# Kernel tuning notes

Hardware: AMD Instinct MI355X
Metric: run time of the kernel (lower is better)

The kernel has to match this reference:

```python
import jax, jax.numpy as jnp
from jax import lax
import numpy as np

REACH = 4
NPRED = 4
NBINS = 256


def _conv(x, w, groups=1):
    # NCHW valid conv
    return lax.conv_general_dilated(
        x, w, window_strides=(1, 1), padding='VALID',
        dimension_numbers=('NCHW', 'OIHW', 'NCHW'),
        feature_group_count=groups)


def _median3(a, b, c):
    return jnp.maximum(jnp.minimum(a, jnp.maximum(b, c)), jnp.minimum(b, c))


def _calc_rmse(x):
    return 255.0 * jnp.sqrt(jnp.mean(jnp.square(x)))


def _calc_invCR(x):
    # torch.histc(x, 256, -1, 1) per (batch, channel) slice, then Shannon entropy
    b, c, h, w = x.shape
    nch = b * c
    res = h * w
    xf = x.reshape(nch, res)
    valid = ((xf >= -1.0) & (xf <= 1.0)).astype(jnp.float32)  # histc ignores out-of-range
    idx = jnp.clip(jnp.floor((xf + 1.0) * (NBINS / 2.0)).astype(jnp.int32), 0, NBINS - 1)
    flat = (jnp.arange(nch, dtype=jnp.int32)[:, None] * NBINS + idx).reshape(-1)
    counts = jnp.zeros(nch * NBINS, jnp.float32).at[flat].add(valid.reshape(-1))
    prob = counts / res
    ent = jnp.sum(jnp.where(prob > 0, -prob * jnp.log2(jnp.where(prob > 0, prob, 1.0)), 0.0))
    return ent / (8.0 * nch)


def _forward(x, w0T, w0L, b0L, w1, b1, w2, b2):
    r, g, b = x[:, 0:1], x[:, 1:2], x[:, 2:3]
    yuv = jnp.concatenate([r - g, g, b - g], axis=1)  # [B,3,H,W]
    # conv0T: causal-north context, pad (left=4, right=4, top=4) on rows [:-1]
    padT = jnp.pad(yuv[:, :, :-1, :], ((0, 0), (0, 0), (REACH, 0), (REACH, REACH)))
    # conv0L: causal-west context, pad left=4 on cols [:-1]
    padL = jnp.pad(yuv[:, :, :, :-1], ((0, 0), (0, 0), (0, 0), (REACH, 0)))
    pred = jax.nn.leaky_relu(_conv(padT, w0T) + _conv(padL, w0L) + b0L[None, :, None, None])
    # grouped 1x1 mixing back to 3 channels (conv1, conv2; groups=3)
    pred = jax.nn.leaky_relu(_conv(pred, w1, groups=3) + b1[None, :, None, None])
    pred = _conv(pred, w2, groups=3) + b2[None, :, None, None]  # [B,3,H,W]
    north = jnp.pad(yuv[:, :, :-1, :], ((0, 0), (0, 0), (1, 0), (0, 0)))
    west = jnp.pad(yuv[:, :, :, :-1], ((0, 0), (0, 0), (0, 0), (1, 0)))
    northeast = jnp.pad(yuv[:, :, :-1, 1:], ((0, 0), (0, 0), (1, 0), (0, 1)))
    vmin = jnp.minimum(west, jnp.minimum(north, northeast))
    vmax = jnp.maximum(west, jnp.maximum(north, northeast))
    pred = _median3(pred, vmin, vmax)
    pcr, py, pcb = pred[:, 0:1], pred[:, 1:2], pred[:, 2:3]
    pred = jnp.concatenate([pcr + g, py, pcb + g], axis=1)
    pred = jnp.clip(pred, -1.0, 1.0)
    delta = x - pred
    return delta


def setup_inputs() -> dict:
    key = jax.random.key(0)
    ks = jax.random.split(key, 9)
    B, H, W = 16, 512, 512
    x = jax.random.uniform(ks[0], (B, 3, H, W), jnp.float32) * 2.0 - 1.0
    s = 0.05
    return {
        'x': x,
        'w0T': jax.random.normal(ks[1], (3 * NPRED, 3, REACH, 2 * REACH + 1), jnp.float32) * s,
        'w0L': jax.random.normal(ks[2], (3 * NPRED, 3, 1, REACH), jnp.float32) * s,
        'b0L': jax.random.normal(ks[3], (3 * NPRED,), jnp.float32) * s,
        'w1': jax.random.normal(ks[4], (3 * NPRED, NPRED, 1, 1), jnp.float32) * s,
        'b1': jax.random.normal(ks[5], (3 * NPRED,), jnp.float32) * s,
        'w2': jax.random.normal(ks[6], (3, NPRED, 1, 1), jnp.float32) * s,
        'b2': jax.random.normal(ks[7], (3,), jnp.float32) * s,
    }


def reference(x, w0T, w0L, b0L, w1, b1, w2, b2):
    delta = _forward(x, w0T, w0L, b0L, w1, b1, w2, b2)
    loss1 = _calc_rmse(delta)
    loss0 = _calc_rmse(x)
    invCR0 = _calc_invCR(x)
    invCR1 = _calc_invCR(jnp.fmod(delta + 1.0, 2.0) - 1.0)
    return (loss1, loss0, invCR0, invCR1)
```

## Files before the change

### kernel.cpp

```cpp
#include <hip/hip_runtime.h>
#include <math.h>

constexpr int TH = 16, TW = 64;
constexpr int LH = TH + 4, LW = TW + 8;

typedef __attribute__((ext_vector_type(8))) short bf16x8;
typedef __attribute__((ext_vector_type(4))) float f32x4;

__device__ __forceinline__ float leaky(float v){ return v >= 0.0f ? v : 0.01f * v; }

__device__ __forceinline__ unsigned cvt_pk_bf16(float lo, float hi){
  unsigned r;
  asm("v_cvt_pk_bf16_f32 %0, %1, %2" : "=v"(r) : "v"(lo), "v"(hi));
  return r;
}

__global__ void codec_zero(unsigned int* ws, int n){
  int i = blockIdx.x * 256 + threadIdx.x;
  if (i < n) ws[i] = 0u;
}

__global__ __launch_bounds__(256) void codec_main(
    const float* __restrict__ x,
    const float* __restrict__ w0T, const float* __restrict__ w0L,
    const float* __restrict__ b0L,
    const float* __restrict__ w1, const float* __restrict__ b1,
    const float* __restrict__ w2, const float* __restrict__ b2,
    unsigned int* __restrict__ histX, unsigned int* __restrict__ histD,
    float* __restrict__ sums)
{
  __shared__ float yuv[3][LH][LW];
  __shared__ __attribute__((aligned(16))) float h0buf[4][4][16][16];
  __shared__ unsigned int lhX[3][256];
  __shared__ unsigned int lhD[3][256];
  __shared__ float red[2];

  const int tid  = threadIdx.x;
  const int lane = tid & 63;
  const int wv   = tid >> 6;
  const int p    = lane & 15;
  const int g    = lane >> 4;

  const int b  = blockIdx.z;
  const int h0 = blockIdx.y * TH;
  const int w0 = blockIdx.x * TW;

  bf16x8 afrag[4];
  #pragma unroll
  for (int t = 0; t < 4; ++t){
    float wv8[8];
    #pragma unroll
    for (int e = 0; e < 8; ++e){
      float v = 0.0f;
      if (p < 12){
        if (t < 3)          v = w0T[p*108 + t*36 + g*9 + e];
        else if (g < 3)     v = (e < 4) ? w0L[p*12 + g*4 + e]
                                        : w0T[p*108 + g*36 + (e-4)*9 + 8];
      }
      wv8[e] = v;
    }
    union { unsigned u[4]; bf16x8 s; } pk;
    #pragma unroll
    for (int i = 0; i < 4; ++i) pk.u[i] = cvt_pk_bf16(wv8[2*i], wv8[2*i+1]);
    afrag[t] = pk.s;
  }

  for (int i = tid; i < 3*256; i += 256){ (&lhX[0][0])[i] = 0u; (&lhD[0][0])[i] = 0u; }
  if (tid < 2) red[tid] = 0.0f;

  const float* xb = x + (size_t)b * (3*512*512);
  for (int i = tid; i < LH*LW; i += 256){
    int lr = i / LW, lc = i % LW;
    int h = h0 + lr - 4, w = w0 + lc - 4;
    float r = 0.f, gg = 0.f, bb = 0.f;
    if (h >= 0 && w >= 0 && w < 512){
      int off = h*512 + w;
      r  = xb[off];
      gg = xb[262144 + off];
      bb = xb[524288 + off];
    }
    yuv[0][lr][lc] = r - gg;
    yuv[1][lr][lc] = gg;
    yuv[2][lr][lc] = bb - gg;
  }
  __syncthreads();

  float lsq_d = 0.0f, lsq_x = 0.0f;

  for (int qi = 0; qi < 4; ++qi){
    const int row = wv*4 + qi;
    const int lr  = row + 4;

    for (int s = 0; s < 4; ++s){
      const int lc = 4 + s*16 + p;
      f32x4 acc = {0.f, 0.f, 0.f, 0.f};
      #pragma unroll
      for (int t = 0; t < 4; ++t){
        float f[8];
        if (t < 3){
          const float* src = &yuv[t][lr-4+g][lc-4];
          #pragma unroll
          for (int i = 0; i < 8; ++i) f[i] = src[i];
        } else {
          const int ic = (g < 3) ? g : 2;
          const float* L = &yuv[ic][lr][lc-4];
          #pragma unroll
          for (int i = 0; i < 4; ++i) f[i] = L[i];
          #pragma unroll
          for (int dy = 0; dy < 4; ++dy) f[4+dy] = yuv[ic][lr-4+dy][lc+4];
        }
        union { unsigned u[4]; bf16x8 s_; } pk;
        #pragma unroll
        for (int i = 0; i < 4; ++i) pk.u[i] = cvt_pk_bf16(f[2*i], f[2*i+1]);
        acc = __builtin_amdgcn_mfma_f32_16x16x32_bf16(afrag[t], pk.s_, acc, 0, 0, 0);
      }
      *(f32x4*)&h0buf[wv][s][p][g*4] = acc;
    }

    const int colp = lane;
    const int lc2  = colp + 4;
    f32x4 r0 = *(const f32x4*)&h0buf[wv][colp>>4][colp&15][0];
    f32x4 r1 = *(const f32x4*)&h0buf[wv][colp>>4][colp&15][4];
    f32x4 r2 = *(const f32x4*)&h0buf[wv][colp>>4][colp&15][8];
    float h0v[12] = { r0[0], r0[1], r0[2], r0[3],
                      r1[0], r1[1], r1[2], r1[3],
                      r2[0], r2[1], r2[2], r2[3] };
    #pragma unroll
    for (int oc = 0; oc < 12; ++oc) h0v[oc] = leaky(h0v[oc] + b0L[oc]);

    float h1v[12];
    #pragma unroll
    for (int j = 0; j < 12; ++j){
      int gsel = (j >> 2) << 2;
      float sv = b1[j];
      #pragma unroll
      for (int k = 0; k < 4; ++k) sv = fmaf(w1[j*4+k], h0v[gsel+k], sv);
      h1v[j] = leaky(sv);
    }
    float pr2[3];
    #pragma unroll
    for (int c = 0; c < 3; ++c){
      float sv = b2[c];
      #pragma unroll
      for (int k = 0; k < 4; ++k) sv = fmaf(w2[c*4+k], h1v[c*4+k], sv);
      pr2[c] = sv;
    }

    const float gpix = yuv[1][lr][lc2];
    const int h = h0 + row;
    const int w = w0 + colp;
    const int off = h*512 + w;

    #pragma unroll
    for (int c = 0; c < 3; ++c){
      float n  = yuv[c][lr-1][lc2];
      float wl = yuv[c][lr][lc2-1];
      float ne = yuv[c][lr-1][lc2+1];
      float vmin = fminf(wl, fminf(n, ne));
      float vmax = fmaxf(wl, fmaxf(n, ne));
      float pv = fminf(fmaxf(pr2[c], vmin), vmax);
      pv = (c == 1) ? pv : pv + gpix;
      pv = fminf(fmaxf(pv, -1.0f), 1.0f);

      float xv = xb[c*262144 + off];
      float d  = xv - pv;
      lsq_d = fmaf(d, d, lsq_d);
      lsq_x = fmaf(xv, xv, lsq_x);

      int ix = (int)floorf((xv + 1.0f) * 128.0f);
      ix = ix < 0 ? 0 : (ix > 255 ? 255 : ix);
      if (xv >= -1.0f && xv <= 1.0f) atomicAdd(&lhX[c][ix], 1u);

      float wd = fmodf(d + 1.0f, 2.0f) - 1.0f;
      int id = (int)floorf((wd + 1.0f) * 128.0f);
      id = id < 0 ? 0 : (id > 255 ? 255 : id);
      if (wd >= -1.0f && wd <= 1.0f) atomicAdd(&lhD[c][id], 1u);
    }
  }

  #pragma unroll
  for (int sft = 32; sft > 0; sft >>= 1){
    lsq_d += __shfl_down(lsq_d, sft);
    lsq_x += __shfl_down(lsq_x, sft);
  }
  if ((tid & 63) == 0){ atomicAdd(&red[0], lsq_d); atomicAdd(&red[1], lsq_x); }
  __syncthreads();
  if (tid == 0){ atomicAdd(&sums[0], red[0]); atomicAdd(&sums[1], red[1]); }

  for (int i = tid; i < 3*256; i += 256){
    int c = i >> 8, bin = i & 255;
    unsigned vX = lhX[c][bin];
    if (vX) atomicAdd(&histX[(b*3 + c)*256 + bin], vX);
    unsigned vD = lhD[c][bin];
    if (vD) atomicAdd(&histD[(b*3 + c)*256 + bin], vD);
  }
}

__global__ __launch_bounds__(256) void codec_final(
    const unsigned int* __restrict__ histX,
    const unsigned int* __restrict__ histD,
    const float* __restrict__ sums,
    float* __restrict__ out)
{
  __shared__ float se[2];
  if (threadIdx.x < 2) se[threadIdx.x] = 0.0f;
  __syncthreads();
  float eX = 0.0f, eD = 0.0f;
  for (int i = threadIdx.x; i < 48*256; i += 256){
    float pX = (float)histX[i] * (1.0f/262144.0f);
    if (pX > 0.0f) eX -= pX * log2f(pX);
    float pD = (float)histD[i] * (1.0f/262144.0f);
    if (pD > 0.0f) eD -= pD * log2f(pD);
  }
  #pragma unroll
  for (int s = 32; s > 0; s >>= 1){
    eX += __shfl_down(eX, s);
    eD += __shfl_down(eD, s);
  }
  if ((threadIdx.x & 63) == 0){ atomicAdd(&se[0], eX); atomicAdd(&se[1], eD); }
  __syncthreads();
  if (threadIdx.x == 0){
    out[0] = 255.0f * sqrtf(sums[0] * (1.0f/12582912.0f));
    out[1] = 255.0f * sqrtf(sums[1] * (1.0f/12582912.0f));
    out[2] = se[0] * (1.0f/384.0f);
    out[3] = se[1] * (1.0f/384.0f);
  }
}

extern "C" void kernel_launch(void* const* d_in, const int* in_sizes, int n_in,
                              void* d_out, int out_size, void* d_ws, size_t ws_size,
                              hipStream_t stream) {
  const float* x   = (const float*)d_in[0];
  const float* w0T = (const float*)d_in[1];
  const float* w0L = (const float*)d_in[2];
  const float* b0L = (const float*)d_in[3];
  const float* w1  = (const float*)d_in[4];
  const float* b1  = (const float*)d_in[5];
  const float* w2  = (const float*)d_in[6];
  const float* b2  = (const float*)d_in[7];

  unsigned int* histX = (unsigned int*)d_ws;
  unsigned int* histD = histX + 48*256;
  float* sums = (float*)(histD + 48*256);
  float* out = (float*)d_out;

  const int nzero = 48*256*2 + 2;
  codec_zero<<<(nzero + 255)/256, 256, 0, stream>>>((unsigned int*)d_ws, nzero);

  dim3 grid(512/TW, 512/TH, 16);
  codec_main<<<grid, 256, 0, stream>>>(x, w0T, w0L, b0L, w1, b1, w2, b2,
                                       histX, histD, sums);
  codec_final<<<1, 256, 0, stream>>>(histX, histD, sums, out);
}
```

Baseline: 239.3 us.

## Pre-pack bf16 tile pairs in LDS and run epilogue directly from MFMA accumulators

Adds a shared-memory pass that converts the YUV tile to packed bf16 pairs, one copy per column parity, so MFMA B-fragments become four dword loads instead of eight float loads plus conversions. The h0buf round-trip through LDS is removed: each MFMA output lane group now holds exactly one channel's four hidden values and finishes the grouped 1x1 mixes, median clamp, loss and histogram work itself. Per-group weights are hoisted into registers. The costs are an extra LDS conversion pass and sync, and a quarter of the lanes (g==3) sit idle during the epilogue.

```diff
diff --git a/kernel.cpp b/kernel.cpp
--- a/kernel.cpp
+++ b/kernel.cpp
@@ -3,6 +3,10 @@
 
 constexpr int TH = 16, TW = 64;
 constexpr int LH = TH + 4, LW = TW + 8;
+constexpr int PLS = LH*LW + 8;
+constexpr int PKW = LW/2;
+constexpr int PKPL = LH*PKW;
+constexpr int PKPAR = 3*PKPL;
 
 typedef __attribute__((ext_vector_type(8))) short bf16x8;
 typedef __attribute__((ext_vector_type(4))) float f32x4;
@@ -29,8 +33,8 @@
     unsigned int* __restrict__ histX, unsigned int* __restrict__ histD,
     float* __restrict__ sums)
 {
-  __shared__ float yuv[3][LH][LW];
-  __shared__ __attribute__((aligned(16))) float h0buf[4][4][16][16];
+  __shared__ float yuvF[3*PLS];
+  __shared__ unsigned pkF[2*PKPAR];
   __shared__ unsigned int lhX[3][256];
   __shared__ unsigned int lhD[3][256];
   __shared__ float red[2];
@@ -40,10 +44,13 @@
   const int wv   = tid >> 6;
   const int p    = lane & 15;
   const int g    = lane >> 4;
+  const int gg   = (g < 3) ? g : 0;
 
   const int b  = blockIdx.z;
   const int h0 = blockIdx.y * TH;
   const int w0 = blockIdx.x * TW;
+
+#define YUV(t, r, c) yuvF[(t)*PLS + (r)*LW + (c)]
 
   bf16x8 afrag[4];
   #pragma unroll
@@ -65,6 +72,19 @@
     afrag[t] = pk.s;
   }
 
+  float b0g[4], b1g[4], w2g[4], w1g[4][4];
+  #pragma unroll
+  for (int k = 0; k < 4; ++k){
+    b0g[k] = b0L[4*gg + k];
+    b1g[k] = b1[4*gg + k];
+    w2g[k] = w2[gg*4 + k];
+  }
+  #pragma unroll
+  for (int jj = 0; jj < 4; ++jj)
+    #pragma unroll
+    for (int k = 0; k < 4; ++k) w1g[jj][k] = w1[(4*gg + jj)*4 + k];
+  const float b2g = b2[gg];
+
   for (int i = tid; i < 3*256; i += 256){ (&lhX[0][0])[i] = 0u; (&lhD[0][0])[i] = 0u; }
   if (tid < 2) red[tid] = 0.0f;
 
@@ -72,16 +92,26 @@
   for (int i = tid; i < LH*LW; i += 256){
     int lr = i / LW, lc = i % LW;
     int h = h0 + lr - 4, w = w0 + lc - 4;
-    float r = 0.f, gg = 0.f, bb = 0.f;
+    float r = 0.f, ggv = 0.f, bb = 0.f;
     if (h >= 0 && w >= 0 && w < 512){
       int off = h*512 + w;
-      r  = xb[off];
-      gg = xb[262144 + off];
-      bb = xb[524288 + off];
+      r   = xb[off];
+      ggv = xb[262144 + off];
+      bb  = xb[524288 + off];
     }
-    yuv[0][lr][lc] = r - gg;
-    yuv[1][lr][lc] = gg;
-    yuv[2][lr][lc] = bb - gg;
+    YUV(0, lr, lc) = r - ggv;
+    YUV(1, lr, lc) = ggv;
+    YUV(2, lr, lc) = bb - ggv;
+  }
+  __syncthreads();
+
+  for (int i = tid; i < 2*PKPAR; i += 256){
+    int par = i / PKPAR, rem = i % PKPAR;
+    int pl = rem / PKPL, r2 = (rem % PKPL) / PKW, wd = rem % PKW;
+    int c0 = 2*wd + par, c1 = c0 + 1;
+    float lo = YUV(pl, r2, c0);
+    float hi = (c1 < LW) ? YUV(pl, r2, c1) : 0.0f;
+    pkF[i] = cvt_pk_bf16(lo, hi);
   }
   __syncthreads();
 
@@ -92,89 +122,72 @@
     const int lr  = row + 4;
 
     for (int s = 0; s < 4; ++s){
-      const int lc = 4 + s*16 + p;
+      const int c0    = s*16 + p;
+      const int par   = c0 & 1;
+      const int wbase = (c0 - par) >> 1;
       f32x4 acc = {0.f, 0.f, 0.f, 0.f};
+
       #pragma unroll
       for (int t = 0; t < 4; ++t){
-        float f[8];
+        union { unsigned u[4]; bf16x8 v; } B;
         if (t < 3){
-          const float* src = &yuv[t][lr-4+g][lc-4];
+          const unsigned* src = &pkF[par*PKPAR + t*PKPL + (lr-4+g)*PKW + wbase];
           #pragma unroll
-          for (int i = 0; i < 8; ++i) f[i] = src[i];
+          for (int i = 0; i < 4; ++i) B.u[i] = src[i];
         } else {
           const int ic = (g < 3) ? g : 2;
-          const float* L = &yuv[ic][lr][lc-4];
+          const unsigned* L = &pkF[par*PKPAR + ic*PKPL + lr*PKW + wbase];
+          B.u[0] = L[0]; B.u[1] = L[1];
+          float f4 = YUV(ic, lr-4+0, c0+8);
+          float f5 = YUV(ic, lr-4+1, c0+8);
+          float f6 = YUV(ic, lr-4+2, c0+8);
+          float f7 = YUV(ic, lr-4+3, c0+8);
+          B.u[2] = cvt_pk_bf16(f4, f5);
+          B.u[3] = cvt_pk_bf16(f6, f7);
+        }
+        acc = __builtin_amdgcn_mfma_f32_16x16x32_bf16(afrag[t], B.v, acc, 0, 0, 0);
+      }
+
+      if (g < 3){
+        const int lc = c0 + 4;
+        float h0v[4], h1v[4];
+        #pragma unroll
+        for (int k = 0; k < 4; ++k) h0v[k] = leaky(acc[k] + b0g[k]);
+        #pragma unroll
+        for (int jj = 0; jj < 4; ++jj){
+          float sv = b1g[jj];
           #pragma unroll
-          for (int i = 0; i < 4; ++i) f[i] = L[i];
-          #pragma unroll
-          for (int dy = 0; dy < 4; ++dy) f[4+dy] = yuv[ic][lr-4+dy][lc+4];
+          for (int k = 0; k < 4; ++k) sv = fmaf(w1g[jj][k], h0v[k], sv);
+          h1v[jj] = leaky(sv);
         }
-        union { unsigned u[4]; bf16x8 s_; } pk;
+        float pr = b2g;
         #pragma unroll
-        for (int i = 0; i < 4; ++i) pk.u[i] = cvt_pk_bf16(f[2*i], f[2*i+1]);
-        acc = __builtin_amdgcn_mfma_f32_16x16x32_bf16(afrag[t], pk.s_, acc, 0, 0, 0);
+        for (int k = 0; k < 4; ++k) pr = fmaf(w2g[k], h1v[k], pr);
+
+        float n  = YUV(g, lr-1, lc);
+        float wl = YUV(g, lr,   lc-1);
+        float ne = YUV(g, lr-1, lc+1);
+        float vmin = fminf(wl, fminf(n, ne));
+        float vmax = fmaxf(wl, fmaxf(n, ne));
+        float pv = fminf(fmaxf(pr, vmin), vmax);
+        float gpix = YUV(1, lr, lc);
+        pv = (g == 1) ? pv : pv + gpix;
+        pv = fminf(fmaxf(pv, -1.0f), 1.0f);
+
+        float xv = xb[g*262144 + (h0+row)*512 + (w0 + s*16 + p)];
+        float d  = xv - pv;
+        lsq_d = fmaf(d, d, lsq_d);
+        lsq_x = fmaf(xv, xv, lsq_x);
+
+        int ix = (int)floorf((xv + 1.0f) * 128.0f);
+        ix = ix < 0 ? 0 : (ix > 255 ? 255 : ix);
+        if (xv >= -1.0f && xv <= 1.0f) atomicAdd(&lhX[g][ix], 1u);
+
+        float wd2 = fmodf(d + 1.0f, 2.0f) - 1.0f;
+        int id = (int)floorf((wd2 + 1.0f) * 128.0f);
+        id = id < 0 ? 0 : (id > 255 ? 255 : id);
+        if (wd2 >= -1.0f && wd2 <= 1.0f) atomicAdd(&lhD[g][id], 1u);
       }
-      *(f32x4*)&h0buf[wv][s][p][g*4] = acc;
-    }
-
-    const int colp = lane;
-    const int lc2  = colp + 4;
-    f32x4 r0 = *(const f32x4*)&h0buf[wv][colp>>4][colp&15][0];
-    f32x4 r1 = *(const f32x4*)&h0buf[wv][colp>>4][colp&15][4];
-    f32x4 r2 = *(const f32x4*)&h0buf[wv][colp>>4][colp&15][8];
-    float h0v[12] = { r0[0], r0[1], r0[2], r0[3],
-                      r1[0], r1[1], r1[2], r1[3],
-                      r2[0], r2[1], r2[2], r2[3] };
-    #pragma unroll
-    for (int oc = 0; oc < 12; ++oc) h0v[oc] = leaky(h0v[oc] + b0L[oc]);
-
-    float h1v[12];
-    #pragma unroll
-    for (int j = 0; j < 12; ++j){
-      int gsel = (j >> 2) << 2;
-      float sv = b1[j];
-      #pragma unroll
-      for (int k = 0; k < 4; ++k) sv = fmaf(w1[j*4+k], h0v[gsel+k], sv);
-      h1v[j] = leaky(sv);
-    }
-    float pr2[3];
-    #pragma unroll
-    for (int c = 0; c < 3; ++c){
-      float sv = b2[c];
-      #pragma unroll
-      for (int k = 0; k < 4; ++k) sv = fmaf(w2[c*4+k], h1v[c*4+k], sv);
-      pr2[c] = sv;
-    }
-
-    const float gpix = yuv[1][lr][lc2];
-    const int h = h0 + row;
-    const int w = w0 + colp;
-    const int off = h*512 + w;
-
-    #pragma unroll
-    for (int c = 0; c < 3; ++c){
-      float n  = yuv[c][lr-1][lc2];
-      float wl = yuv[c][lr][lc2-1];
-      float ne = yuv[c][lr-1][lc2+1];
-      float vmin = fminf(wl, fminf(n, ne));
-      float vmax = fmaxf(wl, fmaxf(n, ne));
-      float pv = fminf(fmaxf(pr2[c], vmin), vmax);
-      pv = (c == 1) ? pv : pv + gpix;
-      pv = fminf(fmaxf(pv, -1.0f), 1.0f);
-
-      float xv = xb[c*262144 + off];
-      float d  = xv - pv;
-      lsq_d = fmaf(d, d, lsq_d);
-      lsq_x = fmaf(xv, xv, lsq_x);
-
-      int ix = (int)floorf((xv + 1.0f) * 128.0f);
-      ix = ix < 0 ? 0 : (ix > 255 ? 255 : ix);
-      if (xv >= -1.0f && xv <= 1.0f) atomicAdd(&lhX[c][ix], 1u);
-
-      float wd = fmodf(d + 1.0f, 2.0f) - 1.0f;
-      int id = (int)floorf((wd + 1.0f) * 128.0f);
-      id = id < 0 ? 0 : (id > 255 ? 255 : id);
-      if (wd >= -1.0f && wd <= 1.0f) atomicAdd(&lhD[c][id], 1u);
     }
   }
 
@@ -194,6 +207,7 @@
     unsigned vD = lhD[c][bin];
     if (vD) atomicAdd(&histD[(b*3 + c)*256 + bin], vD);
   }
+#undef YUV
 }
 
 __global__ __launch_bounds__(256) void codec_final(
```

Result: no change. 238.4 us (-0.4%).
